# Kernel tuning notes

Measured on AMD Instinct MI355X. Metric: run time of the kernel, lower is better.

## Reference

```python
import jax, jax.numpy as jnp
import numpy as np

WAVE_LEN = 1000.0
DIM_G = 64


def box_relational_embedding(boxes):
    # boxes: (B, N, 4) -> (B, N, N, 64) trigonometric geometry embedding
    B, N, _ = boxes.shape
    x_min, y_min, x_max, y_max = jnp.split(boxes, 4, axis=-1)  # each (B,N,1)
    cx = (x_min + x_max) * 0.5
    cy = (y_min + y_max) * 0.5
    w = (x_max - x_min) + 1.0
    h = (y_max - y_min) + 1.0
    cxT = jnp.swapaxes(cx, 1, 2)  # (B,1,N)
    cyT = jnp.swapaxes(cy, 1, 2)
    dx = jnp.log(jnp.clip(jnp.abs((cx - cxT) / w), 1e-3))  # (B,N,N)
    dy = jnp.log(jnp.clip(jnp.abs((cy - cyT) / h), 1e-3))
    dw = jnp.log(w / jnp.swapaxes(w, 1, 2))
    dh = jnp.log(h / jnp.swapaxes(h, 1, 2))
    pos = jnp.stack([dx, dy, dw, dh], axis=-1)  # (B,N,N,4)
    n_freq = DIM_G // 8  # 8 frequency bands
    dim_mat = 1.0 / (WAVE_LEN ** (jnp.arange(n_freq, dtype=pos.dtype) / n_freq))
    mul = (100.0 * pos)[..., None] * dim_mat  # (B,N,N,4,8)
    mul = mul.reshape(B, N, N, 4 * n_freq)  # (B,N,N,32)
    return jnp.concatenate([jnp.sin(mul), jnp.cos(mul)], axis=-1)  # (B,N,N,64)


def setup_inputs() -> dict:
    key = jax.random.key(0)
    ks = jax.random.split(key, 12)
    B, N, D, H = 32, 196, 1024, 8
    scale = 0.02
    inp = {
        "input_query": jax.random.normal(ks[0], (B, N, D), jnp.float32),
        "input_key": jax.random.normal(ks[1], (B, N, D), jnp.float32),
        "input_value": jax.random.normal(ks[2], (B, N, D), jnp.float32),
        "input_box": jax.random.uniform(ks[3], (B, N, 4), jnp.float32),
        "Wq": jax.random.normal(ks[4], (D, D), jnp.float32) * scale,
        "bq": jnp.zeros((D,), jnp.float32),
        "Wk": jax.random.normal(ks[5], (D, D), jnp.float32) * scale,
        "bk": jnp.zeros((D,), jnp.float32),
        "Wv": jax.random.normal(ks[6], (D, D), jnp.float32) * scale,
        "bv": jnp.zeros((D,), jnp.float32),
        "Wo": jax.random.normal(ks[7], (D, D), jnp.float32) * scale,
        "bo": jnp.zeros((D,), jnp.float32),
        "WG_w": jax.random.normal(ks[8], (H, DIM_G), jnp.float32) * scale,  # 8 stacked (64->1) linears
        "WG_b": jnp.zeros((H,), jnp.float32),
    }
    return inp


def reference(input_query, input_key, input_value, input_box,
              Wq, bq, Wk, bk, Wv, bv, Wo, bo, WG_w, WG_b):
    B, N, D = input_query.shape
    H = WG_w.shape[0]
    dk = D // H
    # relation geometry weights per head: (B,H,N,N)
    geo = box_relational_embedding(input_box)  # (B,N,N,64)
    wg = jax.nn.relu(jnp.einsum('bnmg,hg->bhnm', geo, WG_w) + WG_b[None, :, None, None])
    # projections (torch Linear: x @ W.T + b), reshape to (B,H,N,dk)
    def proj(x, W, b):
        return (x @ W.T + b).reshape(B, N, H, dk).transpose(0, 2, 1, 3)
    q = proj(input_query, Wq, bq)
    k = proj(input_key, Wk, bk)
    v = proj(input_value, Wv, bv)
    scores = jnp.einsum('bhnd,bhmd->bhnm', q, k) / np.sqrt(dk).astype(q.dtype)
    logits = jnp.log(jnp.clip(wg, 1e-6)) + scores
    attn = jax.nn.softmax(logits, axis=-1)  # (B,H,N,N)
    out = jnp.einsum('bhnm,bhmd->bhnd', attn, v)  # (B,H,N,dk)
    out = out.transpose(0, 2, 1, 3).reshape(B, N, D)
    return out @ Wo.T + bo
```

## Files before the change

### kernel.cpp

```cpp
#include <hip/hip_runtime.h>
#include <hip/hip_bf16.h>

typedef __bf16 bf16;
typedef _Float16 half_t;
typedef bf16 bf16x8 __attribute__((ext_vector_type(8)));
typedef bf16 bf16x4 __attribute__((ext_vector_type(4)));
typedef float floatx4 __attribute__((ext_vector_type(4)));

#define B_ 32
#define N_ 196
#define H_ 8
#define D_ 1024
#define DK_ 128
#define BN_ (B_ * N_)
#define BH_ (B_ * H_)
#define NPAD_ 224
#define PSTRIDE_ 232

#define KT_ 16

typedef __attribute__((address_space(3))) unsigned int lds_uint;
typedef const __attribute__((address_space(1))) unsigned int glb_uint;

__device__ __forceinline__ void async_copy16(const bf16* g, bf16* l) {
  __builtin_amdgcn_global_load_lds((glb_uint*)g, (lds_uint*)l, 16, 0, 0);
}

#define BARRIER() asm volatile("s_barrier" ::: "memory")
#define WAITV0() asm volatile("s_waitcnt vmcnt(0)" ::: "memory")

__global__ __launch_bounds__(256) void cvt3_kernel(const float* __restrict__ s0,
                                                   const float* __restrict__ s1,
                                                   const float* __restrict__ s2,
                                                   bf16* __restrict__ d0,
                                                   bf16* __restrict__ d1,
                                                   bf16* __restrict__ d2, int n4) {
  const int which = blockIdx.y;
  const float* s = (which == 0) ? s0 : (which == 1) ? s1 : s2;
  bf16* d = (which == 0) ? d0 : (which == 1) ? d1 : d2;
  int i = blockIdx.x * 256 + threadIdx.x;
  if (i >= n4) return;
  float4 v = ((const float4*)s)[i];
  bf16x4 o;
  o[0] = (bf16)v.x;
  o[1] = (bf16)v.y;
  o[2] = (bf16)v.z;
  o[3] = (bf16)v.w;
  *(bf16x4*)(d + (size_t)i * 4) = o;
}

__global__ __launch_bounds__(256) void cvt4_kernel(const float* __restrict__ s0,
                                                   const float* __restrict__ s1,
                                                   const float* __restrict__ s2,
                                                   const float* __restrict__ s3,
                                                   bf16* __restrict__ d0,
                                                   bf16* __restrict__ d1,
                                                   bf16* __restrict__ d2,
                                                   bf16* __restrict__ d3, int n4) {
  const int which = blockIdx.y;
  const float* s = (which == 0) ? s0 : (which == 1) ? s1 : (which == 2) ? s2 : s3;
  bf16* d = (which == 0) ? d0 : (which == 1) ? d1 : (which == 2) ? d2 : d3;
  int i = blockIdx.x * 256 + threadIdx.x;
  if (i >= n4) return;
  float4 v = ((const float4*)s)[i];
  bf16x4 o;
  o[0] = (bf16)v.x;
  o[1] = (bf16)v.y;
  o[2] = (bf16)v.z;
  o[3] = (bf16)v.w;
  *(bf16x4*)(d + (size_t)i * 4) = o;
}

__global__ __launch_bounds__(256) void geo_kernel(const float* __restrict__ box,
                                                  const float* __restrict__ WGw,
                                                  const float* __restrict__ WGb,
                                                  half_t* __restrict__ S) {
  __shared__ float4 wsh[128];
  if (threadIdx.x < 128) wsh[threadIdx.x] = ((const float4*)WGw)[threadIdx.x];
  __syncthreads();

  int tid = blockIdx.x * 256 + threadIdx.x;
  int b = tid / (N_ * N_);
  int rem = tid - b * (N_ * N_);
  int n = rem / N_;
  int m = rem - n * N_;

  float4 bn = ((const float4*)box)[b * N_ + n];
  float4 bm = ((const float4*)box)[b * N_ + m];
  float cxn = (bn.x + bn.z) * 0.5f, cyn = (bn.y + bn.w) * 0.5f;
  float wn = bn.z - bn.x + 1.0f, hn = bn.w - bn.y + 1.0f;
  float cxm = (bm.x + bm.z) * 0.5f, cym = (bm.y + bm.w) * 0.5f;
  float wm = bm.z - bm.x + 1.0f, hm = bm.w - bm.y + 1.0f;

  float pos[4];
  pos[0] = __logf(fmaxf(fabsf((cxn - cxm) / wn), 1e-3f));
  pos[1] = __logf(fmaxf(fabsf((cyn - cym) / hn), 1e-3f));
  pos[2] = __logf(wn / wm);
  pos[3] = __logf(hn / hm);

  const float dims[8] = {1.0f,          0.4216965034f, 0.1778279410f, 0.0749894209f,
                         0.0316227766f, 0.0133352143f, 0.0056234133f, 0.0023713737f};
  float feat[64];
#pragma unroll
  for (int p = 0; p < 4; p++) {
#pragma unroll
    for (int f = 0; f < 8; f++) {
      float a = 100.0f * pos[p] * dims[f];
      feat[p * 8 + f] = __sinf(a);
      feat[32 + p * 8 + f] = __cosf(a);
    }
  }
#pragma unroll
  for (int hh = 0; hh < 8; hh++) {
    float accv = WGb[hh];
#pragma unroll
    for (int g4 = 0; g4 < 16; g4++) {
      float4 wv = wsh[hh * 16 + g4];
      accv += feat[g4 * 4 + 0] * wv.x + feat[g4 * 4 + 1] * wv.y +
              feat[g4 * 4 + 2] * wv.z + feat[g4 * 4 + 3] * wv.w;
    }
    S[((size_t)((b * H_ + hh) * N_ + n)) * NPAD_ + m] = (half_t)fmaxf(accv, 1e-6f);
  }
}

template <int VARIANT>
__global__ __launch_bounds__(256, 2) void gemm2p(
    const bf16* __restrict__ A0, const bf16* __restrict__ A1, const bf16* __restrict__ A2,
    const bf16* __restrict__ W0, const bf16* __restrict__ W1, const bf16* __restrict__ W2,
    const float* __restrict__ b0, const float* __restrict__ b1, const float* __restrict__ b2,
    void* __restrict__ O0, void* __restrict__ O1, void* __restrict__ O2) {
  __shared__ bf16 As[2][128 * 64];
  __shared__ bf16 Bs[2][128 * 64];

  const int NZ = (VARIANT == 0) ? 3 : 1;
  const int chunk = 49 * NZ;
  const int f = blockIdx.x + (blockIdx.y << 3) + blockIdx.z * 392;
  const int L = (f & 7) * chunk + (f >> 3);
  const int lx = L & 7;
  const int lyz = L >> 3;
  const int ly = (VARIANT == 0) ? (lyz % 49) : lyz;
  const int z = (VARIANT == 0) ? (lyz / 49) : 0;

  const bf16* A = (z == 0) ? A0 : (z == 1) ? A1 : A2;
  const bf16* W = (z == 0) ? W0 : (z == 1) ? W1 : W2;
  const float* bias = (z == 0) ? b0 : (z == 1) ? b1 : b2;

  const int tid = threadIdx.x;
  const int lane = tid & 63;
  const int wid = tid >> 6;
  const int l16 = lane & 15;
  const int quad = lane >> 4;
  const int wm = wid >> 1;
  const int wn = wid & 1;

  const bf16* gA = A + (size_t)ly * 128 * D_;
  const bf16* gB = W + (size_t)lx * 128 * D_;

  const int srow = tid >> 3;
  const int lslot = (tid & 7) ^ (srow & 7);
  size_t sOff[4];
#pragma unroll
  for (int u = 0; u < 4; u++) sOff[u] = (size_t)(u * 32 + srow) * D_ + lslot * 8;

  int arow[4], brow[4], kslot[2];
#pragma unroll
  for (int i = 0; i < 4; i++) arow[i] = (wm * 64 + i * 16 + l16) * 64;
#pragma unroll
  for (int j = 0; j < 4; j++) brow[j] = (wn * 64 + j * 16 + l16) * 64;
#pragma unroll
  for (int kk = 0; kk < 2; kk++) kslot[kk] = ((kk * 4 + quad) ^ (l16 & 7)) * 8;

  floatx4 acc[4][4];
#pragma unroll
  for (int i = 0; i < 4; i++)
#pragma unroll
    for (int j = 0; j < 4; j++)
#pragma unroll
      for (int r = 0; r < 4; r++) acc[i][j][r] = 0.0f;

#pragma unroll
  for (int u = 0; u < 4; u++) {
    async_copy16(gA + sOff[u], &As[0][u * 2048 + tid * 8]);
    async_copy16(gB + sOff[u], &Bs[0][u * 2048 + tid * 8]);
  }
  WAITV0();
  BARRIER();

  for (int kt = 0; kt < KT_; ++kt) {
    const int cur = kt & 1;
    const bf16* Ab = As[cur];
    const bf16* Bb = Bs[cur];
    const bool pf = (kt + 1 < KT_);
    const bf16* pa = gA + (kt + 1) * 64;
    const bf16* pb = gB + (kt + 1) * 64;
    bf16* dA = As[cur ^ 1];
    bf16* dB = Bs[cur ^ 1];
    bf16x8 af[4], bfv[4];

#pragma unroll
    for (int i = 0; i < 4; i++) af[i] = *(const bf16x8*)(Ab + arow[i] + kslot[0]);
#pragma unroll
    for (int j = 0; j < 4; j++) bfv[j] = *(const bf16x8*)(Bb + brow[j] + kslot[0]);
    if (pf) {
#pragma unroll
      for (int u = 0; u < 4; u++) async_copy16(pa + sOff[u], dA + u * 2048 + tid * 8);
    }
    __builtin_amdgcn_s_setprio(1);
#pragma unroll
    for (int i = 0; i < 4; i++)
#pragma unroll
      for (int j = 0; j < 4; j++)
        acc[i][j] = __builtin_amdgcn_mfma_f32_16x16x32_bf16(af[i], bfv[j], acc[i][j], 0, 0, 0);
    __builtin_amdgcn_s_setprio(0);

#pragma unroll
    for (int i = 0; i < 4; i++) af[i] = *(const bf16x8*)(Ab + arow[i] + kslot[1]);
#pragma unroll
    for (int j = 0; j < 4; j++) bfv[j] = *(const bf16x8*)(Bb + brow[j] + kslot[1]);
    if (pf) {
#pragma unroll
      for (int u = 0; u < 4; u++) async_copy16(pb + sOff[u], dB + u * 2048 + tid * 8);
    }
    __builtin_amdgcn_s_setprio(1);
#pragma unroll
    for (int i = 0; i < 4; i++)
#pragma unroll
      for (int j = 0; j < 4; j++)
        acc[i][j] = __builtin_amdgcn_mfma_f32_16x16x32_bf16(af[i], bfv[j], acc[i][j], 0, 0, 0);
    __builtin_amdgcn_s_setprio(0);

    if (pf) {
      WAITV0();
      BARRIER();
    }
  }

  const int m0 = ly * 128 + wm * 64;
  const int n0 = lx * 128 + wn * 64;
#pragma unroll
  for (int j = 0; j < 4; j++) {
    const int col = n0 + j * 16 + l16;
    const float bv = bias[col];
#pragma unroll
    for (int i = 0; i < 4; i++) {
#pragma unroll
      for (int r = 0; r < 4; r++) {
        const int row = m0 + i * 16 + quad * 4 + r;
        float v = acc[i][j][r] + bv;
        if (VARIANT == 1) {
          ((float*)O0)[(size_t)row * D_ + col] = v;
        } else if (z < 2) {
          bf16* Cout = z ? (bf16*)O1 : (bf16*)O0;
          Cout[(size_t)row * D_ + col] = (bf16)v;
        } else {
          int b = row / N_;
          int n = row - b * N_;
          int h = col >> 7;
          int d = col & (DK_ - 1);
          ((bf16*)O2)[((size_t)((b * H_ + h) * DK_ + d)) * NPAD_ + n] = (bf16)v;
        }
      }
    }
  }
}

__global__ __launch_bounds__(256) void attn_kernel(const bf16* __restrict__ Q,
                                                   const bf16* __restrict__ Kmat,
                                                   const bf16* __restrict__ Vt,
                                                   const half_t* __restrict__ Sb,
                                                   bf16* __restrict__ AO) {
  __shared__ alignas(16) char smem[46080];
  bf16* KsB[2] = {(bf16*)smem, (bf16*)smem + 4096};
  bf16* Pl = (bf16*)smem;
  bf16* VsB[2] = {(bf16*)(smem + 29696), (bf16*)(smem + 29696) + 4096};

  const int f = blockIdx.x;
  const int tile = (f >> 3) & 3;
  const int bh = (f & 7) | ((f >> 5) << 3);
  const int b = bh >> 3;
  const int h = bh & 7;
  const int tid = threadIdx.x;
  const int wave = tid >> 6;
  const int lane = tid & 63;
  const int l16 = lane & 15;
  const int quad = lane >> 4;
  const int nrb = tile * 64 + wave * 16;

  size_t kSrc[2];
  int kDst[2];
#pragma unroll
  for (int u = 0; u < 2; u++) {
    const int slot = u * 256 + tid;
    const int srow = slot >> 4;
    const int scs = slot & 15;
    kSrc[u] = (size_t)(b * N_ + srow) * D_ + h * DK_ + (scs ^ (srow & 7)) * 8;
    kDst[u] = slot * 8;
  }
  size_t vSrc[2];
#pragma unroll
  for (int u = 0; u < 2; u++) {
    const int slot = u * 256 + tid;
    const int vrow = slot >> 2;
    const int vcs = slot & 3;
    vSrc[u] = (size_t)bh * DK_ * NPAD_ + (size_t)vrow * NPAD_ + (vcs ^ (vrow & 3)) * 8;
  }

#pragma unroll
  for (int u = 0; u < 2; u++) async_copy16(Kmat + kSrc[u], KsB[0] + kDst[u]);

  const int na = nrb + l16;
  const bool nav = na < N_;
  const bf16* aptr = Q + ((size_t)(b * N_ + (nav ? na : 0))) * D_ + h * DK_ + quad * 8;
  bf16x8 afr[4];
#pragma unroll
  for (int kk = 0; kk < 4; kk++) {
    bf16x8 v = *(const bf16x8*)(aptr + kk * 32);
    if (!nav) {
#pragma unroll
      for (int e = 0; e < 8; e++) v[e] = (bf16)0.0f;
    }
    afr[kk] = v;
  }
  WAITV0();
  BARRIER();

  floatx4 S[14];
#pragma unroll
  for (int j = 0; j < 14; j++)
#pragma unroll
    for (int r = 0; r < 4; r++) S[j][r] = 0.0f;

  for (int jt = 0; jt < 7; ++jt) {
    const int cur = jt & 1;
    if (jt < 6) {
      const size_t koff = (size_t)((jt + 1) * 32) * D_;
#pragma unroll
      for (int u = 0; u < 2; u++)
        async_copy16(Kmat + kSrc[u] + koff, KsB[cur ^ 1] + kDst[u]);
    }
    const bf16* Kb = KsB[cur];
    __builtin_amdgcn_s_setprio(1);
#pragma unroll
    for (int jj = 0; jj < 2; jj++) {
      const int mloc = jj * 16 + l16;
#pragma unroll
      for (int kk = 0; kk < 4; kk++) {
        bf16x8 bb = *(const bf16x8*)(Kb + mloc * 128 + ((kk * 4 + quad) ^ (l16 & 7)) * 8);
        S[jt * 2 + jj] = __builtin_amdgcn_mfma_f32_16x16x32_bf16(afr[kk], bb, S[jt * 2 + jj], 0, 0, 0);
      }
    }
    __builtin_amdgcn_s_setprio(0);
    if (jt < 6) {
      WAITV0();
      BARRIER();
    }
  }

#pragma unroll
  for (int u = 0; u < 2; u++) async_copy16(Vt + vSrc[u], VsB[0] + kDst[u]);

  BARRIER();

  const float scale = 0.08838834764831845f;
  const half_t* bbase = Sb + ((size_t)bh * N_) * NPAD_;
  bf16* pw = Pl + wave * 16 * PSTRIDE_;
  float inv[4];
#pragma unroll
  for (int r = 0; r < 4; r++) {
    const int n = nrb + quad * 4 + r;
    const bool nv = n < N_;
    const size_t brow = (size_t)(nv ? n : 0) * NPAD_;
    float mx = -1e30f;
#pragma unroll
    for (int j = 0; j < 14; j++) {
      const int m = j * 16 + l16;
      float s = (nv && m < N_) ? S[j][r] * scale : -1e30f;
      S[j][r] = s;
      mx = fmaxf(mx, s);
    }
#pragma unroll
    for (int off = 1; off < 16; off <<= 1) mx = fmaxf(mx, __shfl_xor(mx, off, 64));
    float sum = 0.0f;
#pragma unroll
    for (int j = 0; j < 14; j++) {
      const int m = j * 16 + l16;
      float w = (m < N_) ? (float)bbase[brow + m] : 0.0f;
      float e = w * __expf(S[j][r] - mx);
      sum += e;
      pw[(quad * 4 + r) * PSTRIDE_ + m] = (bf16)e;
    }
#pragma unroll
    for (int off = 1; off < 16; off <<= 1) sum += __shfl_xor(sum, off, 64);
    inv[r] = 1.0f / sum;
  }
  __syncthreads();

  floatx4 O[8];
#pragma unroll
  for (int j2 = 0; j2 < 8; j2++)
#pragma unroll
    for (int r = 0; r < 4; r++) O[j2][r] = 0.0f;

  const bf16* pr = pw + l16 * PSTRIDE_ + quad * 8;
  for (int t7 = 0; t7 < 7; ++t7) {
    const int cur = t7 & 1;
    if (t7 < 6) {
      const size_t voff = (size_t)((t7 + 1) * 32);
#pragma unroll
      for (int u = 0; u < 2; u++)
        async_copy16(Vt + vSrc[u] + voff, VsB[cur ^ 1] + kDst[u]);
    }
    const bf16* Vb = VsB[cur];
    bf16x8 a = *(const bf16x8*)(pr + t7 * 32);
    __builtin_amdgcn_s_setprio(1);
#pragma unroll
    for (int j2 = 0; j2 < 8; j2++) {
      bf16x8 bb = *(const bf16x8*)(Vb + (j2 * 16 + l16) * 32 + (quad ^ (l16 & 3)) * 8);
      O[j2] = __builtin_amdgcn_mfma_f32_16x16x32_bf16(a, bb, O[j2], 0, 0, 0);
    }
    __builtin_amdgcn_s_setprio(0);
    if (t7 < 6) {
      WAITV0();
      BARRIER();
    }
  }

#pragma unroll
  for (int r = 0; r < 4; r++) {
    const int n = nrb + quad * 4 + r;
    if (n < N_) {
#pragma unroll
      for (int j2 = 0; j2 < 8; j2++) {
        AO[((size_t)(b * N_ + n)) * D_ + h * DK_ + j2 * 16 + l16] = (bf16)(O[j2][r] * inv[r]);
      }
    }
  }
}

extern "C" void kernel_launch(void* const* d_in, const int* in_sizes, int n_in,
                              void* d_out, int out_size, void* d_ws, size_t ws_size,
                              hipStream_t stream) {
  const float* xq = (const float*)d_in[0];
  const float* xk = (const float*)d_in[1];
  const float* xv = (const float*)d_in[2];
  const float* box = (const float*)d_in[3];
  const float* Wq = (const float*)d_in[4];
  const float* bq = (const float*)d_in[5];
  const float* Wk = (const float*)d_in[6];
  const float* bk = (const float*)d_in[7];
  const float* Wv = (const float*)d_in[8];
  const float* bv = (const float*)d_in[9];
  const float* Wo = (const float*)d_in[10];
  const float* bo = (const float*)d_in[11];
  const float* WGw = (const float*)d_in[12];
  const float* WGb = (const float*)d_in[13];

  size_t off = 0;
  char* wsc = (char*)d_ws;
  auto alloc = [&](size_t bytes) -> void* {
    void* p = wsc + off;
    off += (bytes + 255) & ~(size_t)255;
    return p;
  };
  bf16* xq_b = (bf16*)alloc((size_t)BN_ * D_ * 2);
  bf16* xk_b = (bf16*)alloc((size_t)BN_ * D_ * 2);
  bf16* xv_b = (bf16*)alloc((size_t)BN_ * D_ * 2);
  bf16* wq_b = (bf16*)alloc((size_t)D_ * D_ * 2);
  bf16* wk_b = (bf16*)alloc((size_t)D_ * D_ * 2);
  bf16* wv_b = (bf16*)alloc((size_t)D_ * D_ * 2);
  bf16* wo_b = (bf16*)alloc((size_t)D_ * D_ * 2);
  bf16* q_b = (bf16*)alloc((size_t)BN_ * D_ * 2);
  bf16* k_b = (bf16*)alloc((size_t)BN_ * D_ * 2);
  bf16* vt_b = (bf16*)alloc((size_t)BH_ * DK_ * NPAD_ * 2);
  bf16* ao_b = (bf16*)alloc((size_t)BN_ * D_ * 2);
  half_t* S = (half_t*)alloc((size_t)BH_ * N_ * NPAD_ * 2);

  const int n4x = BN_ * D_ / 4;
  const int n4w = D_ * D_ / 4;
  dim3 g3(n4x / 256, 3, 1);
  cvt3_kernel<<<g3, 256, 0, stream>>>(xq, xk, xv, xq_b, xk_b, xv_b, n4x);
  dim3 g4(n4w / 256, 4, 1);
  cvt4_kernel<<<g4, 256, 0, stream>>>(Wq, Wk, Wv, Wo, wq_b, wk_b, wv_b, wo_b, n4w);

  geo_kernel<<<(B_ * N_ * N_) / 256, 256, 0, stream>>>(box, WGw, WGb, S);

  hipMemsetAsync(vt_b, 0, (size_t)BH_ * DK_ * NPAD_ * 2, stream);

  dim3 gqkv(D_ / 128, BN_ / 128, 3);
  gemm2p<0><<<gqkv, 256, 0, stream>>>(xq_b, xk_b, xv_b, wq_b, wk_b, wv_b, bq, bk, bv,
                                      q_b, k_b, vt_b);

  attn_kernel<<<1024, 256, 0, stream>>>(q_b, k_b, vt_b, S, ao_b);

  dim3 gout(D_ / 128, BN_ / 128, 1);
  gemm2p<1><<<gout, 256, 0, stream>>>(ao_b, nullptr, nullptr, wo_b, nullptr, nullptr,
                                      bo, nullptr, nullptr, d_out, nullptr, nullptr);
}
```

Measured before the change: 315.0 us.

## Load full K/V per head into LDS once and loop over query tiles

The attention kernel now launches one block per (batch, head) instead of four blocks per head. Each block loads the whole K and V tile for that head into LDS up front, then iterates over the four 64-row query tiles, so K/V are read from global memory once per head rather than once per query tile. This gives up grid parallelism (256 blocks instead of 1024) and needs much more LDS per block (about 144 KB), which lowers occupancy and drops the double-buffered load/compute overlap. Each wave reuses only its own rows of the P buffer across iterations, so no cross-wave barrier is needed there.

```diff
diff --git a/kernel.cpp b/kernel.cpp
--- a/kernel.cpp
+++ b/kernel.cpp
@@ -269,14 +269,11 @@
                                                    const bf16* __restrict__ Vt,
                                                    const half_t* __restrict__ Sb,
                                                    bf16* __restrict__ AO) {
-  __shared__ alignas(16) char smem[46080];
-  bf16* KsB[2] = {(bf16*)smem, (bf16*)smem + 4096};
-  bf16* Pl = (bf16*)smem;
-  bf16* VsB[2] = {(bf16*)(smem + 29696), (bf16*)(smem + 29696) + 4096};
-
-  const int f = blockIdx.x;
-  const int tile = (f >> 3) & 3;
-  const int bh = (f & 7) | ((f >> 5) << 3);
+  __shared__ bf16 Ks[7 * 4096];
+  __shared__ bf16 Vs[7 * 4096];
+  __shared__ bf16 Pl[4 * 16 * PSTRIDE_];
+
+  const int bh = blockIdx.x;
   const int b = bh >> 3;
   const int h = bh & 7;
   const int tid = threadIdx.x;
@@ -284,7 +281,6 @@
   const int lane = tid & 63;
   const int l16 = lane & 15;
   const int quad = lane >> 4;
-  const int nrb = tile * 64 + wave * 16;
 
   size_t kSrc[2];
   int kDst[2];
@@ -306,132 +302,120 @@
   }
 
 #pragma unroll
-  for (int u = 0; u < 2; u++) async_copy16(Kmat + kSrc[u], KsB[0] + kDst[u]);
-
-  const int na = nrb + l16;
-  const bool nav = na < N_;
-  const bf16* aptr = Q + ((size_t)(b * N_ + (nav ? na : 0))) * D_ + h * DK_ + quad * 8;
-  bf16x8 afr[4];
-#pragma unroll
-  for (int kk = 0; kk < 4; kk++) {
-    bf16x8 v = *(const bf16x8*)(aptr + kk * 32);
-    if (!nav) {
-#pragma unroll
-      for (int e = 0; e < 8; e++) v[e] = (bf16)0.0f;
-    }
-    afr[kk] = v;
+  for (int jt = 0; jt < 7; ++jt) {
+    const size_t koff = (size_t)(jt * 32) * D_;
+#pragma unroll
+    for (int u = 0; u < 2; u++) async_copy16(Kmat + kSrc[u] + koff, Ks + jt * 4096 + kDst[u]);
+  }
+#pragma unroll
+  for (int t7 = 0; t7 < 7; ++t7) {
+#pragma unroll
+    for (int u = 0; u < 2; u++) async_copy16(Vt + vSrc[u] + t7 * 32, Vs + t7 * 4096 + kDst[u]);
   }
   WAITV0();
-  BARRIER();
-
-  floatx4 S[14];
-#pragma unroll
-  for (int j = 0; j < 14; j++)
-#pragma unroll
-    for (int r = 0; r < 4; r++) S[j][r] = 0.0f;
-
-  for (int jt = 0; jt < 7; ++jt) {
-    const int cur = jt & 1;
-    if (jt < 6) {
-      const size_t koff = (size_t)((jt + 1) * 32) * D_;
-#pragma unroll
-      for (int u = 0; u < 2; u++)
-        async_copy16(Kmat + kSrc[u] + koff, KsB[cur ^ 1] + kDst[u]);
-    }
-    const bf16* Kb = KsB[cur];
-    __builtin_amdgcn_s_setprio(1);
-#pragma unroll
-    for (int jj = 0; jj < 2; jj++) {
-      const int mloc = jj * 16 + l16;
-#pragma unroll
-      for (int kk = 0; kk < 4; kk++) {
-        bf16x8 bb = *(const bf16x8*)(Kb + mloc * 128 + ((kk * 4 + quad) ^ (l16 & 7)) * 8);
-        S[jt * 2 + jj] = __builtin_amdgcn_mfma_f32_16x16x32_bf16(afr[kk], bb, S[jt * 2 + jj], 0, 0, 0);
-      }
-    }
-    __builtin_amdgcn_s_setprio(0);
-    if (jt < 6) {
-      WAITV0();
-      BARRIER();
-    }
-  }
-
-#pragma unroll
-  for (int u = 0; u < 2; u++) async_copy16(Vt + vSrc[u], VsB[0] + kDst[u]);
-
   BARRIER();
 
   const float scale = 0.08838834764831845f;
   const half_t* bbase = Sb + ((size_t)bh * N_) * NPAD_;
   bf16* pw = Pl + wave * 16 * PSTRIDE_;
-  float inv[4];
-#pragma unroll
-  for (int r = 0; r < 4; r++) {
-    const int n = nrb + quad * 4 + r;
-    const bool nv = n < N_;
-    const size_t brow = (size_t)(nv ? n : 0) * NPAD_;
-    float mx = -1e30f;
-#pragma unroll
-    for (int j = 0; j < 14; j++) {
-      const int m = j * 16 + l16;
-      float s = (nv && m < N_) ? S[j][r] * scale : -1e30f;
-      S[j][r] = s;
-      mx = fmaxf(mx, s);
-    }
-#pragma unroll
-    for (int off = 1; off < 16; off <<= 1) mx = fmaxf(mx, __shfl_xor(mx, off, 64));
-    float sum = 0.0f;
-#pragma unroll
-    for (int j = 0; j < 14; j++) {
-      const int m = j * 16 + l16;
-      float w = (m < N_) ? (float)bbase[brow + m] : 0.0f;
-      float e = w * __expf(S[j][r] - mx);
-      sum += e;
-      pw[(quad * 4 + r) * PSTRIDE_ + m] = (bf16)e;
-    }
-#pragma unroll
-    for (int off = 1; off < 16; off <<= 1) sum += __shfl_xor(sum, off, 64);
-    inv[r] = 1.0f / sum;
-  }
-  __syncthreads();
-
-  floatx4 O[8];
-#pragma unroll
-  for (int j2 = 0; j2 < 8; j2++)
-#pragma unroll
-    for (int r = 0; r < 4; r++) O[j2][r] = 0.0f;
-
   const bf16* pr = pw + l16 * PSTRIDE_ + quad * 8;
-  for (int t7 = 0; t7 < 7; ++t7) {
-    const int cur = t7 & 1;
-    if (t7 < 6) {
-      const size_t voff = (size_t)((t7 + 1) * 32);
-#pragma unroll
-      for (int u = 0; u < 2; u++)
-        async_copy16(Vt + vSrc[u] + voff, VsB[cur ^ 1] + kDst[u]);
-    }
-    const bf16* Vb = VsB[cur];
-    bf16x8 a = *(const bf16x8*)(pr + t7 * 32);
-    __builtin_amdgcn_s_setprio(1);
-#pragma unroll
-    for (int j2 = 0; j2 < 8; j2++) {
-      bf16x8 bb = *(const bf16x8*)(Vb + (j2 * 16 + l16) * 32 + (quad ^ (l16 & 3)) * 8);
-      O[j2] = __builtin_amdgcn_mfma_f32_16x16x32_bf16(a, bb, O[j2], 0, 0, 0);
-    }
-    __builtin_amdgcn_s_setprio(0);
-    if (t7 < 6) {
-      WAITV0();
-      BARRIER();
-    }
-  }
-
-#pragma unroll
-  for (int r = 0; r < 4; r++) {
-    const int n = nrb + quad * 4 + r;
-    if (n < N_) {
+
+  for (int rt = 0; rt < 4; ++rt) {
+    const int nrb = rt * 64 + wave * 16;
+
+    const int na = nrb + l16;
+    const bool nav = na < N_;
+    const bf16* aptr = Q + ((size_t)(b * N_ + (nav ? na : 0))) * D_ + h * DK_ + quad * 8;
+    bf16x8 afr[4];
+#pragma unroll
+    for (int kk = 0; kk < 4; kk++) {
+      bf16x8 v = *(const bf16x8*)(aptr + kk * 32);
+      if (!nav) {
+#pragma unroll
+        for (int e = 0; e < 8; e++) v[e] = (bf16)0.0f;
+      }
+      afr[kk] = v;
+    }
+
+    floatx4 S[14];
+#pragma unroll
+    for (int j = 0; j < 14; j++)
+#pragma unroll
+      for (int r = 0; r < 4; r++) S[j][r] = 0.0f;
+
+#pragma unroll
+    for (int jt = 0; jt < 7; ++jt) {
+      const bf16* Kb = Ks + jt * 4096;
+      __builtin_amdgcn_s_setprio(1);
+#pragma unroll
+      for (int jj = 0; jj < 2; jj++) {
+        const int mloc = jj * 16 + l16;
+#pragma unroll
+        for (int kk = 0; kk < 4; kk++) {
+          bf16x8 bb = *(const bf16x8*)(Kb + mloc * 128 + ((kk * 4 + quad) ^ (l16 & 7)) * 8);
+          S[jt * 2 + jj] = __builtin_amdgcn_mfma_f32_16x16x32_bf16(afr[kk], bb, S[jt * 2 + jj], 0, 0, 0);
+        }
+      }
+      __builtin_amdgcn_s_setprio(0);
+    }
+
+    float inv[4];
+#pragma unroll
+    for (int r = 0; r < 4; r++) {
+      const int n = nrb + quad * 4 + r;
+      const bool nv = n < N_;
+      const size_t brow = (size_t)(nv ? n : 0) * NPAD_;
+      float mx = -1e30f;
+#pragma unroll
+      for (int j = 0; j < 14; j++) {
+        const int m = j * 16 + l16;
+        float s = (nv && m < N_) ? S[j][r] * scale : -1e30f;
+        S[j][r] = s;
+        mx = fmaxf(mx, s);
+      }
+#pragma unroll
+      for (int off = 1; off < 16; off <<= 1) mx = fmaxf(mx, __shfl_xor(mx, off, 64));
+      float sum = 0.0f;
+#pragma unroll
+      for (int j = 0; j < 14; j++) {
+        const int m = j * 16 + l16;
+        float w = (m < N_) ? (float)bbase[brow + m] : 0.0f;
+        float e = w * __expf(S[j][r] - mx);
+        sum += e;
+        pw[(quad * 4 + r) * PSTRIDE_ + m] = (bf16)e;
+      }
+#pragma unroll
+      for (int off = 1; off < 16; off <<= 1) sum += __shfl_xor(sum, off, 64);
+      inv[r] = 1.0f / sum;
+    }
+
+    floatx4 O[8];
+#pragma unroll
+    for (int j2 = 0; j2 < 8; j2++)
+#pragma unroll
+      for (int r = 0; r < 4; r++) O[j2][r] = 0.0f;
+
+#pragma unroll
+    for (int t7 = 0; t7 < 7; ++t7) {
+      const bf16* Vb = Vs + t7 * 4096;
+      bf16x8 a = *(const bf16x8*)(pr + t7 * 32);
+      __builtin_amdgcn_s_setprio(1);
 #pragma unroll
       for (int j2 = 0; j2 < 8; j2++) {
-        AO[((size_t)(b * N_ + n)) * D_ + h * DK_ + j2 * 16 + l16] = (bf16)(O[j2][r] * inv[r]);
+        bf16x8 bb = *(const bf16x8*)(Vb + (j2 * 16 + l16) * 32 + (quad ^ (l16 & 3)) * 8);
+        O[j2] = __builtin_amdgcn_mfma_f32_16x16x32_bf16(a, bb, O[j2], 0, 0, 0);
+      }
+      __builtin_amdgcn_s_setprio(0);
+    }
+
+#pragma unroll
+    for (int r = 0; r < 4; r++) {
+      const int n = nrb + quad * 4 + r;
+      if (n < N_) {
+#pragma unroll
+        for (int j2 = 0; j2 < 8; j2++) {
+          AO[((size_t)(b * N_ + n)) * D_ + h * DK_ + j2 * 16 + l16] = (bf16)(O[j2][r] * inv[r]);
+        }
       }
     }
   }
@@ -490,7 +474,7 @@
   gemm2p<0><<<gqkv, 256, 0, stream>>>(xq_b, xk_b, xv_b, wq_b, wk_b, wv_b, bq, bk, bv,
                                       q_b, k_b, vt_b);
 
-  attn_kernel<<<1024, 256, 0, stream>>>(q_b, k_b, vt_b, S, ao_b);
+  attn_kernel<<<BH_, 256, 0, stream>>>(q_b, k_b, vt_b, S, ao_b);
 
   dim3 gout(D_ / 128, BN_ / 128, 1);
   gemm2p<1><<<gout, 256, 0, stream>>>(ao_b, nullptr, nullptr, wo_b, nullptr, nullptr,
```

Result: no change. 317.0 us (+0.6%).
